# Kernel tuning notes

Measured on AMD Instinct MI355X. Metric: run time of the kernel, lower is better.

## Reference

```python
import jax, jax.numpy as jnp
import numpy as np

B, S, D, H, F = 2, 2048, 1024, 16, 4096
DH = D // H


def setup_inputs() -> dict:
    key = jax.random.key(0)
    ks = jax.random.split(key, 8)
    scale = 0.02
    def nrm(k, shape):
        return jax.random.normal(k, shape, jnp.float32) * scale
    return {
        "x": jax.random.normal(ks[0], (B, S, D), jnp.float32),
        "ln1_g": jnp.ones((D,), jnp.float32),
        "ln1_b": jnp.zeros((D,), jnp.float32),
        "wq": nrm(ks[1], (D, D)), "bq": jnp.zeros((D,), jnp.float32),
        "wk": nrm(ks[2], (D, D)), "bk": jnp.zeros((D,), jnp.float32),
        "wv": nrm(ks[3], (D, D)), "bv": jnp.zeros((D,), jnp.float32),
        "wo": nrm(ks[4], (D, D)), "bo": jnp.zeros((D,), jnp.float32),
        "ln2_g": jnp.ones((D,), jnp.float32),
        "ln2_b": jnp.zeros((D,), jnp.float32),
        "w1": nrm(ks[5], (D, F)), "b1": jnp.zeros((F,), jnp.float32),
        "w2": nrm(ks[6], (F, D)), "b2": jnp.zeros((D,), jnp.float32),
    }


def _layernorm(x, g, b, eps=1e-5):
    m = jnp.mean(x, axis=-1, keepdims=True)
    v = jnp.var(x, axis=-1, keepdims=True)
    return (x - m) / jnp.sqrt(v + eps) * g + b


def reference(x, ln1_g, ln1_b, wq, bq, wk, bk, wv, bv, wo, bo,
              ln2_g, ln2_b, w1, b1, w2, b2):
    # GPT2Block forward, prefill path (state=None): K/V = ln_1(x), causal mask.
    Bx, Sx, Dx = x.shape
    h = _layernorm(x, ln1_g, ln1_b)

    def heads(t):  # [B,S,D] -> [B,H,S,DH]
        return t.reshape(Bx, Sx, H, DH).transpose(0, 2, 1, 3)

    q = heads(h @ wq + bq)
    k = heads(h @ wk + bk)
    v = heads(h @ wv + bv)

    scores = jnp.einsum('bhqd,bhkd->bhqk', q, k) / jnp.sqrt(jnp.float32(DH))
    # masked_softmax: key position < valid_len (= query_pos+1) kept; else -1e6
    causal = jnp.arange(Sx)[None, :] <= jnp.arange(Sx)[:, None]  # [S,S]
    scores = jnp.where(causal, scores, jnp.float32(-1e6))
    attn_w = jax.nn.softmax(scores, axis=-1)

    o = jnp.einsum('bhqk,bhkd->bhqd', attn_w, v)
    o = o.transpose(0, 2, 1, 3).reshape(Bx, Sx, Dx)
    attn_out = o @ wo + bo

    add1 = x + attn_out  # dropout inactive (eval)
    h2 = _layernorm(add1, ln2_g, ln2_b)
    mlp = jax.nn.gelu(h2 @ w1 + b1, approximate=False) @ w2 + b2
    return add1 + mlp
```

## Files before the change

### kernel.cpp

```cpp
#include <hip/hip_runtime.h>
#include <hip/hip_bf16.h>


#define BDIM 1024
#define SEQ 2048
#define NH 16
#define DHEAD 64
#define FDIM 4096
#define QKVD 3072

typedef __attribute__((ext_vector_type(8))) short short8v;
typedef __attribute__((ext_vector_type(4))) float floatx4;

__device__ __forceinline__ unsigned short f2bf(float f) {
    unsigned int u = __float_as_uint(f);
    unsigned int r = u + 0x7FFFu + ((u >> 16) & 1u);
    return (unsigned short)(r >> 16);
}
__device__ __forceinline__ unsigned int pack2bf(float a, float b) {
    return (unsigned int)f2bf(a) | ((unsigned int)f2bf(b) << 16);
}

__device__ __forceinline__ void load16_lds(const unsigned short* g, short* l) {
    __builtin_amdgcn_global_load_lds((const __attribute__((address_space(1))) void*)g,
                                     (__attribute__((address_space(3))) void*)l, 16, 0, 0);
}

__global__ __launch_bounds__(256) void transpose_all(const float* __restrict__ wq,
                                                     const float* __restrict__ wk,
                                                     const float* __restrict__ wv,
                                                     const float* __restrict__ wo,
                                                     const float* __restrict__ w1,
                                                     const float* __restrict__ w2,
                                                     unsigned short* __restrict__ qkvT,
                                                     unsigned short* __restrict__ woT,
                                                     unsigned short* __restrict__ w1T,
                                                     unsigned short* __restrict__ w2T) {
    const int g = blockIdx.x;
    const float* W;
    unsigned short* Wt;
    int K, N, tx, ty;
    if (g < 4096) {
        const int w = g >> 10, tile = g & 1023;
        tx = tile & 31; ty = tile >> 5; K = 1024; N = 1024;
        W = (w == 0) ? wq : (w == 1) ? wk : (w == 2) ? wv : wo;
        Wt = (w == 3) ? woT : qkvT + (size_t)w * 1024 * 1024;
    } else if (g < 8192) {
        const int tile = g - 4096;
        tx = tile & 127; ty = tile >> 7; K = 1024; N = 4096;
        W = w1; Wt = w1T;
    } else {
        const int tile = g - 8192;
        tx = tile & 31; ty = tile >> 5; K = 4096; N = 1024;
        W = w2; Wt = w2T;
    }
    __shared__ float tile[32][33];
    const int t = threadIdx.x;
    const int r = t >> 3, c4 = (t & 7) * 4;
    const int n0 = tx * 32, k0 = ty * 32;
    float4 p = *(const float4*)(W + (size_t)(k0 + r) * N + n0 + c4);
    tile[r][c4 + 0] = p.x;
    tile[r][c4 + 1] = p.y;
    tile[r][c4 + 2] = p.z;
    tile[r][c4 + 3] = p.w;
    __syncthreads();
    ushort4 ou;
    ou.x = f2bf(tile[c4 + 0][r]);
    ou.y = f2bf(tile[c4 + 1][r]);
    ou.z = f2bf(tile[c4 + 2][r]);
    ou.w = f2bf(tile[c4 + 3][r]);
    *(ushort4*)(Wt + (size_t)(n0 + r) * K + k0 + c4) = ou;
}

__global__ void concat_bias(const float* __restrict__ a, const float* __restrict__ b,
                            const float* __restrict__ c, float* __restrict__ out) {
    int i = blockIdx.x * 256 + threadIdx.x;
    out[i] = (i < 1024) ? a[i] : (i < 2048 ? b[i - 1024] : c[i - 2048]);
}

__global__ __launch_bounds__(256) void ln_kernel(const float* __restrict__ x,
                                                 const float* __restrict__ g,
                                                 const float* __restrict__ bb,
                                                 unsigned short* __restrict__ out) {
    const int row = blockIdx.x;
    const int t = threadIdx.x;
    const int c = t * 4;
    float4 p = *(const float4*)(x + (size_t)row * BDIM + c);
    float s = p.x + p.y + p.z + p.w;
    float sq = p.x * p.x + p.y * p.y + p.z * p.z + p.w * p.w;
    for (int off = 1; off < 64; off <<= 1) {
        s += __shfl_xor(s, off);
        sq += __shfl_xor(sq, off);
    }
    __shared__ float ssum[4], ssq[4];
    const int wave = t >> 6, lane = t & 63;
    if (lane == 0) { ssum[wave] = s; ssq[wave] = sq; }
    __syncthreads();
    s = ssum[0] + ssum[1] + ssum[2] + ssum[3];
    sq = ssq[0] + ssq[1] + ssq[2] + ssq[3];
    const float mean = s * (1.0f / BDIM);
    const float var = sq * (1.0f / BDIM) - mean * mean;
    const float rstd = rsqrtf(var + 1e-5f);
    float4 gg = *(const float4*)(g + c);
    float4 bv = *(const float4*)(bb + c);
    ushort4 o;
    o.x = f2bf((p.x - mean) * rstd * gg.x + bv.x);
    o.y = f2bf((p.y - mean) * rstd * gg.y + bv.y);
    o.z = f2bf((p.z - mean) * rstd * gg.z + bv.z);
    o.w = f2bf((p.w - mean) * rstd * gg.w + bv.w);
    *(ushort4*)(out + (size_t)row * BDIM + c) = o;
}

template <int BN, int RES, int GELU, int OBF16, int QSCALE = 0, int VOUT = 0>
__global__ __launch_bounds__(256, 3) void mfma_gemm(const unsigned short* __restrict__ A,
                                                    const unsigned short* __restrict__ Bt,
                                                    const float* __restrict__ bias,
                                                    const float* __restrict__ res,
                                                    void* __restrict__ Cv,
                                                    unsigned short* __restrict__ vtout,
                                                    int M, int N, int K) {
    constexpr int MI = (BN == 128) ? 4 : 2;
    constexpr int CHB = BN * 4;
    __shared__ short As[2][128 * 32];
    __shared__ short Bs[2][BN * 32];
    const int t = threadIdx.x;
    const int wave = t >> 6, lane = t & 63;
    const int m0 = blockIdx.y * 128, n0 = blockIdx.x * BN;
    const int wmrow = (BN == 128) ? (wave & 1) * 64 : wave * 32;
    const int wnrow = (BN == 128) ? (wave >> 1) * 64 : 0;
    const int mlane = lane & 15, quad = lane >> 4;

    floatx4 acc[MI][4];
#pragma unroll
    for (int mi = 0; mi < MI; ++mi)
#pragma unroll
        for (int ni = 0; ni < 4; ++ni) {
            floatx4 z = {0.0f, 0.0f, 0.0f, 0.0f};
            acc[mi][ni] = z;
        }

    for (int k0 = 0; k0 < K; k0 += 64) {
        __syncthreads();
#pragma unroll
        for (int j = 0; j < 4; ++j) {
            const int c = j * 256 + t;
            const int hh = c >> 9, cc = c & 511;
            load16_lds(A + (size_t)(m0 + (cc >> 2)) * K + k0 + hh * 32 + (cc & 3) * 8,
                       &As[hh][cc * 8]);
        }
#pragma unroll
        for (int j = 0; j < CHB / 128; ++j) {
            const int c = j * 256 + t;
            const int hh = c / CHB, cc = c % CHB;
            load16_lds(Bt + (size_t)(n0 + (cc >> 2)) * K + k0 + hh * 32 + (cc & 3) * 8,
                       &Bs[hh][cc * 8]);
        }
        __syncthreads();
#pragma unroll
        for (int hh = 0; hh < 2; ++hh) {
            short8v a[MI], b[4];
#pragma unroll
            for (int mi = 0; mi < MI; ++mi)
                a[mi] = *(const short8v*)&As[hh][(wmrow + mi * 16 + mlane) * 32 + quad * 8];
#pragma unroll
            for (int ni = 0; ni < 4; ++ni)
                b[ni] = *(const short8v*)&Bs[hh][(wnrow + ni * 16 + mlane) * 32 + quad * 8];
#pragma unroll
            for (int mi = 0; mi < MI; ++mi)
#pragma unroll
                for (int ni = 0; ni < 4; ++ni)
                    acc[mi][ni] = __builtin_amdgcn_mfma_f32_16x16x32_bf16(a[mi], b[ni], acc[mi][ni], 0, 0, 0);
        }
    }
#pragma unroll
    for (int mi = 0; mi < MI; ++mi) {
#pragma unroll
        for (int ni = 0; ni < 4; ++ni) {
            const int col = n0 + wnrow + ni * 16 + mlane;
            const float bv = bias[col];
            const int row0 = m0 + wmrow + mi * 16 + quad * 4;
            if (VOUT && col >= 2048) {
                const int vd = col - 2048;
                const int bb = row0 >> 11, ss = row0 & 2047;
                uint2 pk;
                pk.x = pack2bf(acc[mi][ni][0] + bv, acc[mi][ni][1] + bv);
                pk.y = pack2bf(acc[mi][ni][2] + bv, acc[mi][ni][3] + bv);
                *(uint2*)(vtout + ((size_t)(bb * NH + (vd >> 6)) * DHEAD + (vd & 63)) * SEQ + ss) = pk;
            } else {
#pragma unroll
                for (int rg = 0; rg < 4; ++rg) {
                    const int row = row0 + rg;
                    float v = acc[mi][ni][rg] + bv;
                    if (RES) v += res[(size_t)row * N + col];
                    if (GELU) v = 0.5f * v * (1.0f + erff(v * 0.70710678118654752f));
                    if (QSCALE && col < 1024) v *= 0.125f;
                    if (OBF16)
                        ((unsigned short*)Cv)[(size_t)row * N + col] = f2bf(v);
                    else
                        ((float*)Cv)[(size_t)row * N + col] = v;
                }
            }
        }
    }
}

__global__ __launch_bounds__(256) void attn_kernel(const unsigned short* __restrict__ qkv,
                                                   const unsigned short* __restrict__ vt,
                                                   unsigned short* __restrict__ o) {
    const int g = blockIdx.x;
    const int qt = (g < 256) ? (15 - (g >> 5)) : ((g - 256) >> 5);
    const int hb = g & 31;
    const int h = hb & 15, b = hb >> 4;
    const int t = threadIdx.x;
    const int wave = t >> 6, lane = t & 63;
    const int mlane = lane & 15, quad = lane >> 4;
    const int wq0 = qt * 128 + wave * 32;
    const size_t bS = (size_t)b * SEQ;

    __shared__ unsigned short Ks[64][72];
    __shared__ unsigned short Vs[64][72];
    __shared__ __align__(16) unsigned short plds[4][2][16][72];

    short8v qf[2][2];
#pragma unroll
    for (int ng = 0; ng < 2; ++ng) {
        const unsigned short* qrow = qkv + (bS + wq0 + ng * 16 + mlane) * QKVD + h * DHEAD;
        qf[ng][0] = *(const short8v*)(qrow + quad * 8);
        qf[ng][1] = *(const short8v*)(qrow + 32 + quad * 8);
    }

    const unsigned short* kbase = qkv + bS * QKVD + 1024 + h * DHEAD;
    const unsigned short* vbase = vt + ((size_t)(b * NH + h)) * DHEAD * SEQ;

    const int sr = t >> 3, so = (t & 7) * 8;
    const unsigned short* kg0 = kbase + (size_t)sr * QKVD + so;
    const unsigned short* kg1 = kbase + (size_t)(32 + sr) * QKVD + so;
    const unsigned short* vg0 = vbase + (size_t)sr * SEQ + so;
    const unsigned short* vg1 = vbase + (size_t)(32 + sr) * SEQ + so;

    floatx4 ot[2][4];
#pragma unroll
    for (int ng = 0; ng < 2; ++ng)
#pragma unroll
        for (int mt = 0; mt < 4; ++mt) { floatx4 z = {0, 0, 0, 0}; ot[ng][mt] = z; }
    float m_r[2] = {-INFINITY, -INFINITY}, l_r[2] = {0.0f, 0.0f};

    const int kend = wq0 + 32;
    const int kmax = qt * 128 + 128;

    uint4 kr0 = *(const uint4*)kg0;
    uint4 kr1 = *(const uint4*)kg1;
    uint4 vr0 = *(const uint4*)vg0;
    uint4 vr1 = *(const uint4*)vg1;

    for (int k0 = 0; k0 < kmax; k0 += 64) {
        *(uint4*)&Ks[sr][so] = kr0;
        *(uint4*)&Ks[32 + sr][so] = kr1;
        *(uint4*)&Vs[sr][so] = vr0;
        *(uint4*)&Vs[32 + sr][so] = vr1;
        __syncthreads();
        if (k0 + 64 < kmax) {
            kr0 = *(const uint4*)(kg0 + (size_t)(k0 + 64) * QKVD);
            kr1 = *(const uint4*)(kg1 + (size_t)(k0 + 64) * QKVD);
            vr0 = *(const uint4*)(vg0 + (k0 + 64));
            vr1 = *(const uint4*)(vg1 + (k0 + 64));
        }
        if (k0 < kend) {
            floatx4 st[2][4];
#pragma unroll
            for (int ng = 0; ng < 2; ++ng)
#pragma unroll
                for (int kt = 0; kt < 4; ++kt) {
                    floatx4 mz = {-1e30f, -1e30f, -1e30f, -1e30f};
                    st[ng][kt] = mz;
                }
#pragma unroll
            for (int kt = 0; kt < 4; ++kt) {
                if (k0 + kt * 16 < kend) {
                    short8v kfa = *(const short8v*)&Ks[kt * 16 + mlane][quad * 8];
                    short8v kfb = *(const short8v*)&Ks[kt * 16 + mlane][32 + quad * 8];
#pragma unroll
                    for (int ng = 0; ng < 2; ++ng) {
                        floatx4 z = {0, 0, 0, 0};
                        st[ng][kt] = __builtin_amdgcn_mfma_f32_16x16x32_bf16(kfa, qf[ng][0], z, 0, 0, 0);
                        st[ng][kt] = __builtin_amdgcn_mfma_f32_16x16x32_bf16(kfb, qf[ng][1], st[ng][kt], 0, 0, 0);
                    }
                }
            }
            if (k0 + 64 >= kend) {
#pragma unroll
                for (int ng = 0; ng < 2; ++ng)
#pragma unroll
                    for (int kt = 0; kt < 4; ++kt)
#pragma unroll
                        for (int rg = 0; rg < 4; ++rg)
                            if (k0 + kt * 16 + quad * 4 + rg > wq0 + ng * 16 + mlane)
                                st[ng][kt][rg] = -1e30f;
            }
#pragma unroll
            for (int ng = 0; ng < 2; ++ng) {
                float tm = st[ng][0][0];
#pragma unroll
                for (int kt = 0; kt < 4; ++kt)
#pragma unroll
                    for (int rg = 0; rg < 4; ++rg) tm = fmaxf(tm, st[ng][kt][rg]);
                tm = fmaxf(tm, __shfl_xor(tm, 16));
                tm = fmaxf(tm, __shfl_xor(tm, 32));
                const float newm = fmaxf(m_r[ng], tm);
                const float alpha = __expf(m_r[ng] - newm);
                m_r[ng] = newm;
                float p[4][4], psum = 0.0f;
#pragma unroll
                for (int kt = 0; kt < 4; ++kt)
#pragma unroll
                    for (int rg = 0; rg < 4; ++rg) {
                        p[kt][rg] = __expf(st[ng][kt][rg] - newm);
                        psum += p[kt][rg];
                    }
                psum += __shfl_xor(psum, 16);
                psum += __shfl_xor(psum, 32);
                l_r[ng] = l_r[ng] * alpha + psum;
#pragma unroll
                for (int mt = 0; mt < 4; ++mt)
#pragma unroll
                    for (int rg = 0; rg < 4; ++rg) ot[ng][mt][rg] *= alpha;
#pragma unroll
                for (int kt = 0; kt < 4; ++kt) {
                    uint2 pk;
                    pk.x = pack2bf(p[kt][0], p[kt][1]);
                    pk.y = pack2bf(p[kt][2], p[kt][3]);
                    *(uint2*)&plds[wave][ng][mlane][kt * 16 + quad * 4] = pk;
                }
            }
#pragma unroll
            for (int kh = 0; kh < 2; ++kh) {
                if (k0 + kh * 32 < kend) {
                    short8v vf[4];
#pragma unroll
                    for (int mt = 0; mt < 4; ++mt)
                        vf[mt] = *(const short8v*)&Vs[mt * 16 + mlane][kh * 32 + quad * 8];
#pragma unroll
                    for (int ng = 0; ng < 2; ++ng) {
                        short8v pf = *(const short8v*)&plds[wave][ng][mlane][kh * 32 + quad * 8];
#pragma unroll
                        for (int mt = 0; mt < 4; ++mt)
                            ot[ng][mt] = __builtin_amdgcn_mfma_f32_16x16x32_bf16(vf[mt], pf, ot[ng][mt], 0, 0, 0);
                    }
                }
            }
        }
        __syncthreads();
    }

#pragma unroll
    for (int ng = 0; ng < 2; ++ng) {
        const float inv = 1.0f / l_r[ng];
        unsigned short* orow = o + (bS + wq0 + ng * 16 + mlane) * BDIM + h * DHEAD;
#pragma unroll
        for (int mt = 0; mt < 4; ++mt) {
            uint2 pk;
            pk.x = pack2bf(ot[ng][mt][0] * inv, ot[ng][mt][1] * inv);
            pk.y = pack2bf(ot[ng][mt][2] * inv, ot[ng][mt][3] * inv);
            *(uint2*)(orow + mt * 16 + quad * 4) = pk;
        }
    }
}

extern "C" void kernel_launch(void* const* d_in, const int* in_sizes, int n_in,
                              void* d_out, int out_size, void* d_ws, size_t ws_size,
                              hipStream_t stream) {
    const int M = 2 * SEQ;

    const float* x = (const float*)d_in[0];
    const float* ln1_g = (const float*)d_in[1];
    const float* ln1_b = (const float*)d_in[2];
    const float* wq = (const float*)d_in[3];
    const float* bq = (const float*)d_in[4];
    const float* wk = (const float*)d_in[5];
    const float* bk = (const float*)d_in[6];
    const float* wv = (const float*)d_in[7];
    const float* bv = (const float*)d_in[8];
    const float* wo = (const float*)d_in[9];
    const float* bo = (const float*)d_in[10];
    const float* ln2_g = (const float*)d_in[11];
    const float* ln2_b = (const float*)d_in[12];
    const float* w1 = (const float*)d_in[13];
    const float* b1 = (const float*)d_in[14];
    const float* w2 = (const float*)d_in[15];
    const float* b2 = (const float*)d_in[16];

    char* wsb = (char*)d_ws;
    unsigned short* qkv = (unsigned short*)wsb;
    unsigned short* ffn = (unsigned short*)wsb;
    unsigned short* vt = (unsigned short*)(wsb + (24u << 20));
    unsigned short* hbuf = (unsigned short*)(wsb + (32u << 20));
    float* add1 = (float*)(wsb + (40u << 20));
    unsigned short* h2 = (unsigned short*)(wsb + (56u << 20));
    unsigned short* qkvT = (unsigned short*)(wsb + (64u << 20));
    unsigned short* woT = (unsigned short*)(wsb + (70u << 20));
    unsigned short* w1T = (unsigned short*)(wsb + (72u << 20));
    unsigned short* w2T = (unsigned short*)(wsb + (80u << 20));
    float* bqkv = (float*)(wsb + (88u << 20));

    transpose_all<<<12288, 256, 0, stream>>>(wq, wk, wv, wo, w1, w2, qkvT, woT, w1T, w2T);
    concat_bias<<<12, 256, 0, stream>>>(bq, bk, bv, bqkv);

    ln_kernel<<<M, 256, 0, stream>>>(x, ln1_g, ln1_b, hbuf);

    mfma_gemm<128, 0, 0, 1, 1, 1><<<dim3(QKVD / 128, M / 128), 256, 0, stream>>>(
        hbuf, qkvT, bqkv, nullptr, qkv, vt, M, QKVD, 1024);

    attn_kernel<<<512, 256, 0, stream>>>(qkv, vt, hbuf);

    mfma_gemm<64, 1, 0, 0><<<dim3(1024 / 64, M / 128), 256, 0, stream>>>(
        hbuf, woT, bo, x, add1, nullptr, M, 1024, 1024);

    ln_kernel<<<M, 256, 0, stream>>>(add1, ln2_g, ln2_b, h2);

    mfma_gemm<128, 0, 1, 1><<<dim3(FDIM / 128, M / 128), 256, 0, stream>>>(
        h2, w1T, b1, nullptr, ffn, nullptr, M, FDIM, 1024);

    mfma_gemm<64, 1, 0, 0><<<dim3(1024 / 64, M / 128), 256, 0, stream>>>(
        ffn, w2T, b2, add1, (float*)d_out, nullptr, M, 1024, FDIM);
}
```

Before: 358.3 us.

## Interleave query tiles across eight waves per attention block for causal balance

The attention kernel now launches 256 blocks of 512 threads instead of 512 blocks of 256. Each wave handles a 32-row query tile strided by 8 across the sequence, so every block carries a similar causal workload. Each K/V tile loaded to LDS is reused by 8 waves instead of 4. The cost is that waves with early tiles stay idle while the block keeps iterating to the farthest key, and per-block LDS and register pressure rise.

```diff
diff --git a/kernel.cpp b/kernel.cpp
--- a/kernel.cpp
+++ b/kernel.cpp
@@ -204,22 +204,23 @@
     }
 }
 
-__global__ __launch_bounds__(256) void attn_kernel(const unsigned short* __restrict__ qkv,
-                                                   const unsigned short* __restrict__ vt,
-                                                   unsigned short* __restrict__ o) {
+__global__ __launch_bounds__(512, 4) void attn_kernel(const unsigned short* __restrict__ qkv,
+                                                      const unsigned short* __restrict__ vt,
+                                                      unsigned short* __restrict__ o) {
     const int g = blockIdx.x;
-    const int qt = (g < 256) ? (15 - (g >> 5)) : ((g - 256) >> 5);
-    const int hb = g & 31;
-    const int h = hb & 15, b = hb >> 4;
+    const int bh = g & 31;
+    const int j = g >> 5;
+    const int h = bh & 15, b = bh >> 4;
     const int t = threadIdx.x;
     const int wave = t >> 6, lane = t & 63;
     const int mlane = lane & 15, quad = lane >> 4;
-    const int wq0 = qt * 128 + wave * 32;
+    const int qi = j + 8 * wave;
+    const int wq0 = qi * 32;
     const size_t bS = (size_t)b * SEQ;
 
     __shared__ unsigned short Ks[64][72];
     __shared__ unsigned short Vs[64][72];
-    __shared__ __align__(16) unsigned short plds[4][2][16][72];
+    __shared__ __align__(16) unsigned short plds[8][2][16][72];
 
     short8v qf[2][2];
 #pragma unroll
@@ -230,13 +231,11 @@
     }
 
     const unsigned short* kbase = qkv + bS * QKVD + 1024 + h * DHEAD;
-    const unsigned short* vbase = vt + ((size_t)(b * NH + h)) * DHEAD * SEQ;
+    const unsigned short* vbase = vt + ((size_t)bh) * DHEAD * SEQ;
 
     const int sr = t >> 3, so = (t & 7) * 8;
-    const unsigned short* kg0 = kbase + (size_t)sr * QKVD + so;
-    const unsigned short* kg1 = kbase + (size_t)(32 + sr) * QKVD + so;
-    const unsigned short* vg0 = vbase + (size_t)sr * SEQ + so;
-    const unsigned short* vg1 = vbase + (size_t)(32 + sr) * SEQ + so;
+    const unsigned short* kg = kbase + (size_t)sr * QKVD + so;
+    const unsigned short* vg = vbase + (size_t)sr * SEQ + so;
 
     floatx4 ot[2][4];
 #pragma unroll
@@ -246,24 +245,18 @@
     float m_r[2] = {-INFINITY, -INFINITY}, l_r[2] = {0.0f, 0.0f};
 
     const int kend = wq0 + 32;
-    const int kmax = qt * 128 + 128;
-
-    uint4 kr0 = *(const uint4*)kg0;
-    uint4 kr1 = *(const uint4*)kg1;
-    uint4 vr0 = *(const uint4*)vg0;
-    uint4 vr1 = *(const uint4*)vg1;
+    const int kmax = (((j + 57) * 32) + 63) & ~63;
+
+    uint4 kr = *(const uint4*)kg;
+    uint4 vr = *(const uint4*)vg;
 
     for (int k0 = 0; k0 < kmax; k0 += 64) {
-        *(uint4*)&Ks[sr][so] = kr0;
-        *(uint4*)&Ks[32 + sr][so] = kr1;
-        *(uint4*)&Vs[sr][so] = vr0;
-        *(uint4*)&Vs[32 + sr][so] = vr1;
+        *(uint4*)&Ks[sr][so] = kr;
+        *(uint4*)&Vs[sr][so] = vr;
         __syncthreads();
         if (k0 + 64 < kmax) {
-            kr0 = *(const uint4*)(kg0 + (size_t)(k0 + 64) * QKVD);
-            kr1 = *(const uint4*)(kg1 + (size_t)(k0 + 64) * QKVD);
-            vr0 = *(const uint4*)(vg0 + (k0 + 64));
-            vr1 = *(const uint4*)(vg1 + (k0 + 64));
+            kr = *(const uint4*)(kg + (size_t)(k0 + 64) * QKVD);
+            vr = *(const uint4*)(vg + (k0 + 64));
         }
         if (k0 < kend) {
             floatx4 st[2][4];
@@ -410,7 +403,7 @@
     mfma_gemm<128, 0, 0, 1, 1, 1><<<dim3(QKVD / 128, M / 128), 256, 0, stream>>>(
         hbuf, qkvT, bqkv, nullptr, qkv, vt, M, QKVD, 1024);
 
-    attn_kernel<<<512, 256, 0, stream>>>(qkv, vt, hbuf);
+    attn_kernel<<<256, 512, 0, stream>>>(qkv, vt, hbuf);
 
     mfma_gemm<64, 1, 0, 0><<<dim3(1024 / 64, M / 128), 256, 0, stream>>>(
         hbuf, woT, bo, x, add1, nullptr, M, 1024, 1024);
```

New measurement: 383.2 us. 1.07x slower.
